# Performance work log

Hardware: AMD Instinct MI355X
Metric: run time of the kernel (lower is better)

## Reference

```python
import jax, jax.numpy as jnp
import numpy as np

N_MAP, N_ACT, B, E_PER, D = 131072, 1024, 16, 16384, 128
MAP_PER, ACT_PER = N_MAP // B, N_ACT // B
E = B * E_PER
EPS = 1e-5  # torch GroupNorm default eps


def _gn(x, g, b):
    # GroupNorm(1, C) on [N, C]: per-row normalization over channels
    m = jnp.mean(x, -1, keepdims=True)
    v = jnp.mean((x - m) ** 2, -1, keepdims=True)
    return (x - m) * jax.lax.rsqrt(v + EPS) * g + b


def _lin_gn(x, W, g, b, act=True):
    # LaneGCN Linear: nn.Linear(bias=False) -> GroupNorm(1, n_out) -> optional ReLU
    y = _gn(x @ W.T, g, b)
    return jax.nn.relu(y) if act else y


def setup_inputs() -> dict:
    key = jax.random.key(0)
    keys = iter(jax.random.split(key, 64))
    nrm = lambda shape, s=1.0: jax.random.normal(next(keys), shape, jnp.float32) * s
    uni = lambda shape, s=1.0: jax.random.uniform(next(keys), shape, jnp.float32) * s
    inp = {}
    inp['feat'] = nrm((N_MAP, D))
    inp['turn'] = nrm((N_MAP, 2))
    inp['control'] = uni((N_MAP,))
    inp['intersect'] = uni((N_MAP,))
    inp['map_ctrs'] = uni((N_MAP, 2), 100.0)
    inp['actors'] = nrm((N_ACT, D))
    inp['actor_ctrs'] = uni((N_ACT, 2), 100.0)
    # fixed within-scene edge list (stands in for the distance-threshold nonzero)
    rng = np.random.default_rng(0)
    hi = np.concatenate([rng.integers(b * MAP_PER, (b + 1) * MAP_PER, E_PER) for b in range(B)])
    wi = np.concatenate([rng.integers(b * ACT_PER, (b + 1) * ACT_PER, E_PER) for b in range(B)])
    inp['hi'] = jnp.asarray(hi, jnp.int32)
    inp['wi'] = jnp.asarray(wi, jnp.int32)
    # parameters
    W = lambda *s: nrm(s, 0.02)
    g_ = lambda *s: 1.0 + nrm(s, 0.05)
    b_ = lambda *s: nrm(s, 0.05)
    inp['meta_W'], inp['meta_g'], inp['meta_b'] = W(D, D + 4), g_(D), b_(D)
    inp['dW1'], inp['db1'] = W(2, D, 2), b_(2, D)
    inp['dW2'], inp['dg2'], inp['dbt2'] = W(2, D, D), g_(2, D), b_(2, D)
    inp['qW'], inp['qg'], inp['qb'] = W(2, D, D), g_(2, D), b_(2, D)
    inp['cW1'], inp['cg1'], inp['cb1'] = W(2, D, 3 * D), g_(2, D), b_(2, D)
    inp['cW2'] = W(2, D, D)
    inp['aW'] = W(2, D, D)
    inp['ng_g'], inp['ng_b'] = g_(2, D), b_(2, D)
    inp['lW'], inp['lg'], inp['lb'] = W(2, D, D), g_(2, D), b_(2, D)
    return inp


def reference(feat, turn, control, intersect, map_ctrs, actors, actor_ctrs, hi, wi,
              meta_W, meta_g, meta_b, dW1, db1, dW2, dg2, dbt2, qW, qg, qb,
              cW1, cg1, cb1, cW2, aW, ng_g, ng_b, lW, lg, lb):
    # meta fuse: concat(feat, turn, control, intersect) -> Linear+GN+ReLU
    meta = jnp.concatenate([feat, turn, control[:, None], intersect[:, None]], axis=1)
    feat = _lin_gn(meta, meta_W, meta_g, meta_b)
    for i in range(2):  # two Att blocks
        res = feat
        # dist branch: raw ctr offsets -> Linear(2,n_ctx)+ReLU -> Linear+GN+ReLU
        d = map_ctrs[hi] - actor_ctrs[wi]                       # [E, 2]
        d = jax.nn.relu(d @ dW1[i].T + db1[i])                  # [E, D]
        d = _lin_gn(d, dW2[i], dg2[i], dbt2[i])
        q = _lin_gn(feat[hi], qW[i], qg[i], qb[i])              # query on gathered agts
        c = jnp.concatenate([d, q, actors[wi]], axis=1)         # [E, 3D]
        c = _lin_gn(c, cW1[i], cg1[i], cb1[i])
        c = c @ cW2[i].T                                        # bias-free Linear
        a = feat @ aW[i].T                                      # self path, bias-free
        a = a.at[hi].add(c)                                     # scatter-add messages
        a = jax.nn.relu(_gn(a, ng_g[i], ng_b[i]))
        a = _lin_gn(a, lW[i], lg[i], lb[i], act=False)
        feat = jax.nn.relu(a + res)                             # use_relu=True
    return feat
```

## Files before the change

kernel.cpp:

```cpp
#include <hip/hip_runtime.h>
#include <stdint.h>

typedef unsigned short u16;
typedef __bf16 bf16x8 __attribute__((ext_vector_type(8)));
typedef float f32x4 __attribute__((ext_vector_type(4)));

#define MFMA(a, b, c) __builtin_amdgcn_mfma_f32_16x16x32_bf16(a, b, c, 0, 0, 0)

__device__ __forceinline__ u16 f2bf(float f) {
    union { float f; unsigned u; } v; v.f = f;
    unsigned r = v.u + 0x7fffu + ((v.u >> 16) & 1u);
    return (u16)(r >> 16);
}
__device__ __forceinline__ float bf2f(u16 h) {
    union { unsigned u; float f; } v; v.u = ((unsigned)h) << 16; return v.f;
}
__device__ __forceinline__ bf16x8 as_frag(uint4 u) {
    union { uint4 u; bf16x8 b; } v; v.u = u; return v.b;
}
__device__ __forceinline__ bf16x8 ldg_frag(const u16* p) {
    return as_frag(*reinterpret_cast<const uint4*>(p));
}
__device__ __forceinline__ int rowmap(int t, int i) {
    return 32 * (t >> 1) + 8 * (i >> 2) + 4 * (t & 1) + (i & 3);
}

template <int KT>
__device__ __forceinline__ void gemm_acc(const bf16x8* a, const u16* __restrict__ W, int ldw,
                                         f32x4* acc, int c16, int q4) {
#pragma unroll
    for (int n = 0; n < 8; n++) {
        const u16* wp = W + (size_t)(n * 16 + c16) * ldw + q4 * 8;
#pragma unroll
        for (int k = 0; k < KT; k++) {
            bf16x8 b = ldg_frag(wp + k * 32);
            acc[n] = MFMA(a[k], b, acc[n]);
        }
    }
}

__device__ __forceinline__ void gn_t(f32x4* acc, const float* __restrict__ gb, bool relu, int q4) {
    float s = 0.f, s2 = 0.f;
#pragma unroll
    for (int t = 0; t < 8; t++)
#pragma unroll
        for (int r = 0; r < 4; r++) { float x = acc[t][r]; s += x; s2 = fmaf(x, x, s2); }
    s += __shfl_xor(s, 16, 64); s += __shfl_xor(s, 32, 64);
    s2 += __shfl_xor(s2, 16, 64); s2 += __shfl_xor(s2, 32, 64);
    float mean = s * (1.f / 128.f);
    float var = fmaf(s2, 1.f / 128.f, -mean * mean);
    float rstd = rsqrtf(var + 1e-5f);
#pragma unroll
    for (int t = 0; t < 8; t++) {
        const float4* g4 = reinterpret_cast<const float4*>(gb + (t * 16 + q4 * 4) * 2);
        float4 p01 = g4[0], p23 = g4[1];
        float gv[4] = {p01.x, p01.z, p23.x, p23.z};
        float bv[4] = {p01.y, p01.w, p23.y, p23.w};
#pragma unroll
        for (int r = 0; r < 4; r++) {
            float y = fmaf((acc[t][r] - mean) * rstd, gv[r], bv[r]);
            acc[t][r] = relu ? fmaxf(y, 0.f) : y;
        }
    }
}

__device__ __forceinline__ bf16x8 pack_frag(f32x4 lo, f32x4 hi) {
    union { u16 s[8]; bf16x8 b; } t;
#pragma unroll
    for (int j = 0; j < 4; j++) { t.s[j] = f2bf(lo[j]); t.s[4 + j] = f2bf(hi[j]); }
    return t.b;
}

__device__ __forceinline__ void gn_c(f32x4* acc, const float* __restrict__ g,
                                     const float* __restrict__ b, bool relu, int c16) {
    float gs[8], bs[8];
#pragma unroll
    for (int n = 0; n < 8; n++) { gs[n] = g[n * 16 + c16]; bs[n] = b[n * 16 + c16]; }
#pragma unroll
    for (int r = 0; r < 4; r++) {
        float s = 0.f, s2 = 0.f;
#pragma unroll
        for (int n = 0; n < 8; n++) { float x = acc[n][r]; s += x; s2 = fmaf(x, x, s2); }
#pragma unroll
        for (int m = 1; m < 16; m <<= 1) { s += __shfl_xor(s, m, 64); s2 += __shfl_xor(s2, m, 64); }
        float mean = s * (1.f / 128.f);
        float var = fmaf(s2, 1.f / 128.f, -mean * mean);
        float rstd = rsqrtf(var + 1e-5f);
#pragma unroll
        for (int n = 0; n < 8; n++) {
            float y = fmaf((acc[n][r] - mean) * rstd, gs[n], bs[n]);
            acc[n][r] = relu ? fmaxf(y, 0.f) : y;
        }
    }
}

__global__ __launch_bounds__(256) void k_prep(
    const float* __restrict__ dW2s, const float* __restrict__ qWs, const float* __restrict__ cW1s,
    const float* __restrict__ cW2s, const float* __restrict__ aWs, const float* __restrict__ lWs,
    const float* __restrict__ actors, const float* __restrict__ metaW,
    const float* __restrict__ dW1s, const float* __restrict__ db1s,
    const float* __restrict__ dg2s, const float* __restrict__ dbt2s,
    const float* __restrict__ qgs, const float* __restrict__ qbs,
    const float* __restrict__ cg1s, const float* __restrict__ cb1s,
    u16* __restrict__ o_dW2p, u16* __restrict__ o_qW, u16* __restrict__ o_cW1p,
    u16* __restrict__ o_cW2, u16* __restrict__ o_aW, u16* __restrict__ o_lW,
    u16* __restrict__ o_actb, u16* __restrict__ o_mWf, float* __restrict__ o_mWe,
    float* __restrict__ o_dw1p, float* __restrict__ o_gb) {
    int idx = blockIdx.x * 256 + threadIdx.x;
    if (idx >= 412672) return;
    if (idx < 32768) {
        int i = idx >> 14, rem = idx & 16383, ro = rem >> 7, col = rem & 127;
        o_dW2p[idx] = f2bf(dW2s[i * 16384 + rowmap(ro >> 4, ro & 15) * 128 + col]);
    } else if (idx < 65536) {
        int j = idx - 32768; o_qW[j] = f2bf(qWs[j]);
    } else if (idx < 163840) {
        int j = idx - 65536, i = j / 49152, rem = j - i * 49152, ro = rem / 384, col = rem - ro * 384;
        o_cW1p[j] = f2bf(cW1s[i * 49152 + rowmap(ro >> 4, ro & 15) * 384 + col]);
    } else if (idx < 196608) { int j = idx - 163840; o_cW2[j] = f2bf(cW2s[j]); }
    else if (idx < 229376) { int j = idx - 196608; o_aW[j] = f2bf(aWs[j]); }
    else if (idx < 262144) { int j = idx - 229376; o_lW[j] = f2bf(lWs[j]); }
    else if (idx < 393216) { int j = idx - 262144; o_actb[j] = f2bf(actors[j]); }
    else if (idx < 409600) { int j = idx - 393216; o_mWf[j] = f2bf(metaW[(j >> 7) * 132 + (j & 127)]); }
    else if (idx < 410112) { int j = idx - 409600; o_mWe[j] = metaW[(j >> 2) * 132 + 128 + (j & 3)]; }
    else if (idx < 411136) {
        int j = idx - 410112, i = j >> 9, col = (j >> 2) & 127, t = j & 3;
        float v = (t == 0) ? dW1s[i * 256 + col * 2]
                : (t == 1) ? dW1s[i * 256 + col * 2 + 1]
                : (t == 2) ? db1s[i * 128 + col] : 0.f;
        o_dw1p[j] = v;
    } else {
        int j = idx - 411136;
        int tb = j >> 9, rem = j & 511, i = rem >> 8, q = rem & 255, o = q >> 1, f = q & 1;
        const float* gsrc = (tb == 0) ? dg2s : (tb == 1) ? qgs : cg1s;
        const float* bsrc = (tb == 0) ? dbt2s : (tb == 1) ? qbs : cb1s;
        int src = i * 128 + rowmap(o >> 4, o & 15);
        o_gb[j] = f ? bsrc[src] : gsrc[src];
    }
}

__global__ __launch_bounds__(256) void k_meta(
    const float* __restrict__ feat, const float* __restrict__ turn,
    const float* __restrict__ ctrl, const float* __restrict__ inter,
    const u16* __restrict__ mWf, const float* __restrict__ mWe,
    const float* __restrict__ g, const float* __restrict__ b, u16* __restrict__ out) {
    int lane = threadIdx.x & 63, wv = threadIdx.x >> 6;
    int c16 = lane & 15, q4 = lane >> 4;
    int m0 = (blockIdx.x * 4 + wv) * 16;
    bf16x8 a[4];
    const float* xr = feat + (size_t)(m0 + c16) * 128 + q4 * 8;
#pragma unroll
    for (int k = 0; k < 4; k++) {
        float4 u0 = *reinterpret_cast<const float4*>(xr + k * 32);
        float4 u1 = *reinterpret_cast<const float4*>(xr + k * 32 + 4);
        union { u16 s[8]; bf16x8 b; } t;
        t.s[0] = f2bf(u0.x); t.s[1] = f2bf(u0.y); t.s[2] = f2bf(u0.z); t.s[3] = f2bf(u0.w);
        t.s[4] = f2bf(u1.x); t.s[5] = f2bf(u1.y); t.s[6] = f2bf(u1.z); t.s[7] = f2bf(u1.w);
        a[k] = t.b;
    }
    f32x4 acc[8] = {};
    gemm_acc<4>(a, mWf, 128, acc, c16, q4);
#pragma unroll
    for (int r = 0; r < 4; r++) {
        int row = m0 + q4 * 4 + r;
        float t0 = turn[2 * row], t1 = turn[2 * row + 1];
        float cv = ctrl[row], iv = inter[row];
#pragma unroll
        for (int n = 0; n < 8; n++) {
            int col = n * 16 + c16;
            float4 we = reinterpret_cast<const float4*>(mWe)[col];
            acc[n][r] += t0 * we.x + t1 * we.y + cv * we.z + iv * we.w;
        }
    }
    gn_c(acc, g, b, true, c16);
#pragma unroll
    for (int r = 0; r < 4; r++) {
        size_t row = m0 + q4 * 4 + r;
#pragma unroll
        for (int n = 0; n < 8; n++) out[row * 128 + n * 16 + c16] = f2bf(acc[n][r]);
    }
}

__global__ __launch_bounds__(256) void k_nodeA(
    const u16* __restrict__ featb, const u16* __restrict__ qW, const u16* __restrict__ aW,
    const float* __restrict__ qg, const float* __restrict__ qb,
    u16* __restrict__ q_out, float* __restrict__ a_out) {
    int lane = threadIdx.x & 63, wv = threadIdx.x >> 6;
    int c16 = lane & 15, q4 = lane >> 4;
    int m0 = (blockIdx.x * 4 + wv) * 16;
    bf16x8 a[4];
    const u16* xr = featb + (size_t)(m0 + c16) * 128 + q4 * 8;
#pragma unroll
    for (int k = 0; k < 4; k++) a[k] = ldg_frag(xr + k * 32);
    f32x4 accq[8] = {}, acca[8] = {};
    gemm_acc<4>(a, qW, 128, accq, c16, q4);
    gemm_acc<4>(a, aW, 128, acca, c16, q4);
#pragma unroll
    for (int r = 0; r < 4; r++) {
        size_t row = m0 + q4 * 4 + r;
#pragma unroll
        for (int n = 0; n < 8; n++) a_out[row * 128 + n * 16 + c16] = acca[n][r];
    }
    gn_c(accq, qg, qb, true, c16);
#pragma unroll
    for (int r = 0; r < 4; r++) {
        size_t row = m0 + q4 * 4 + r;
#pragma unroll
        for (int n = 0; n < 8; n++) q_out[row * 128 + n * 16 + c16] = f2bf(accq[n][r]);
    }
}

__global__ __launch_bounds__(256) void k_edge(
    const int* __restrict__ hi, const int* __restrict__ wi,
    const float* __restrict__ mctr, const float* __restrict__ actr,
    const float* __restrict__ dw1p, const u16* __restrict__ dW2p,
    const float* __restrict__ gb_d2,
    const u16* __restrict__ q_node, const u16* __restrict__ actb,
    const u16* __restrict__ cW1p, const float* __restrict__ gb_c1,
    const u16* __restrict__ cW2, float* __restrict__ a_out) {
    int lane = threadIdx.x & 63, wv = threadIdx.x >> 6;
    int c16 = lane & 15, q4 = lane >> 4;
    int bid = (int)blockIdx.x;
    bid = (bid & 7) * 256 + (bid >> 3);
    int ebase = bid * 128 + wv * 32;
    int h0 = hi[ebase + c16], w0 = wi[ebase + c16];
    int h1 = hi[ebase + 16 + c16], w1 = wi[ebase + 16 + c16];
    float dx0 = mctr[2 * h0] - actr[2 * w0], dy0 = mctr[2 * h0 + 1] - actr[2 * w0 + 1];
    float dx1 = mctr[2 * h1] - actr[2 * w1], dy1 = mctr[2 * h1 + 1] - actr[2 * w1 + 1];
    bf16x8 bd0[4], bd1[4];
    const float4* w4p = reinterpret_cast<const float4*>(dw1p);
#pragma unroll
    for (int k = 0; k < 4; k++) {
        union { u16 s[8]; uint4 u; } t0, t1;
#pragma unroll
        for (int j = 0; j < 8; j++) {
            float4 w4 = w4p[k * 32 + q4 * 8 + j];
            t0.s[j] = f2bf(fmaxf(fmaf(dx0, w4.x, fmaf(dy0, w4.y, w4.z)), 0.f));
            t1.s[j] = f2bf(fmaxf(fmaf(dx1, w4.x, fmaf(dy1, w4.y, w4.z)), 0.f));
        }
        bd0[k] = as_frag(t0.u); bd1[k] = as_frag(t1.u);
    }
    f32x4 accA[8] = {}, accB[8] = {};
#pragma unroll
    for (int k = 0; k < 4; k++) {
#pragma unroll
        for (int t = 0; t < 8; t++) {
            bf16x8 a = ldg_frag(dW2p + (size_t)(t * 16 + c16) * 128 + k * 32 + q4 * 8);
            accA[t] = MFMA(a, bd0[k], accA[t]);
            accB[t] = MFMA(a, bd1[k], accB[t]);
        }
    }
    gn_t(accA, gb_d2, true, q4);
    gn_t(accB, gb_d2, true, q4);
    bf16x8 d2f0[4], d2f1[4];
#pragma unroll
    for (int k = 0; k < 4; k++) {
        d2f0[k] = pack_frag(accA[2 * k], accA[2 * k + 1]);
        d2f1[k] = pack_frag(accB[2 * k], accB[2 * k + 1]);
    }
    const u16* qr0 = q_node + (size_t)h0 * 128 + q4 * 8;
    const u16* qr1 = q_node + (size_t)h1 * 128 + q4 * 8;
    const u16* ar0 = actb + (size_t)w0 * 128 + q4 * 8;
    const u16* ar1 = actb + (size_t)w1 * 128 + q4 * 8;
    f32x4 cA[8] = {}, cB[8] = {};
#pragma unroll
    for (int k = 0; k < 12; k++) {
        bf16x8 b0 = (k < 4) ? d2f0[k] : (k < 8) ? ldg_frag(qr0 + (k - 4) * 32)
                                                : ldg_frag(ar0 + (k - 8) * 32);
        bf16x8 b1 = (k < 4) ? d2f1[k] : (k < 8) ? ldg_frag(qr1 + (k - 4) * 32)
                                                : ldg_frag(ar1 + (k - 8) * 32);
#pragma unroll
        for (int t = 0; t < 8; t++) {
            bf16x8 a = ldg_frag(cW1p + (size_t)(t * 16 + c16) * 384 + k * 32 + q4 * 8);
            cA[t] = MFMA(a, b0, cA[t]);
            cB[t] = MFMA(a, b1, cB[t]);
        }
    }
    gn_t(cA, gb_c1, true, q4);
    gn_t(cB, gb_c1, true, q4);
    bf16x8 ba0[4], ba1[4];
#pragma unroll
    for (int k = 0; k < 4; k++) {
        ba0[k] = pack_frag(cA[2 * k], cA[2 * k + 1]);
        ba1[k] = pack_frag(cB[2 * k], cB[2 * k + 1]);
    }
    f32x4 oA[8] = {}, oB[8] = {};
#pragma unroll
    for (int k = 0; k < 4; k++) {
#pragma unroll
        for (int n = 0; n < 8; n++) {
            bf16x8 b = ldg_frag(cW2 + (size_t)(n * 16 + c16) * 128 + k * 32 + q4 * 8);
            oA[n] = MFMA(ba0[k], b, oA[n]);
            oB[n] = MFMA(ba1[k], b, oB[n]);
        }
    }
#pragma unroll
    for (int r = 0; r < 4; r++) {
        int hr0 = hi[ebase + q4 * 4 + r];
        int hr1 = hi[ebase + 16 + q4 * 4 + r];
        float* dst0 = a_out + (size_t)hr0 * 128 + c16;
        float* dst1 = a_out + (size_t)hr1 * 128 + c16;
#pragma unroll
        for (int n = 0; n < 8; n++) {
            unsafeAtomicAdd(dst0 + n * 16, oA[n][r]);
            unsafeAtomicAdd(dst1 + n * 16, oB[n][r]);
        }
    }
}

__global__ __launch_bounds__(256) void k_nodeB(
    const float* __restrict__ a_in, const float* __restrict__ gg, const float* __restrict__ gb,
    const u16* __restrict__ lW, const float* __restrict__ lg, const float* __restrict__ lb,
    const u16* __restrict__ res, u16* __restrict__ out_bf, float* __restrict__ out_f32) {
    int lane = threadIdx.x & 63, wv = threadIdx.x >> 6;
    int c16 = lane & 15, q4 = lane >> 4;
    int m0 = (blockIdx.x * 4 + wv) * 16;
    const float* xr = a_in + (size_t)(m0 + c16) * 128 + q4 * 8;
    float x[32];
#pragma unroll
    for (int k = 0; k < 4; k++) {
        float4 u0 = *reinterpret_cast<const float4*>(xr + k * 32);
        float4 u1 = *reinterpret_cast<const float4*>(xr + k * 32 + 4);
        x[k * 8 + 0] = u0.x; x[k * 8 + 1] = u0.y; x[k * 8 + 2] = u0.z; x[k * 8 + 3] = u0.w;
        x[k * 8 + 4] = u1.x; x[k * 8 + 5] = u1.y; x[k * 8 + 6] = u1.z; x[k * 8 + 7] = u1.w;
    }
    float s = 0.f, s2 = 0.f;
#pragma unroll
    for (int t = 0; t < 32; t++) { s += x[t]; s2 = fmaf(x[t], x[t], s2); }
    s += __shfl_xor(s, 16, 64); s += __shfl_xor(s, 32, 64);
    s2 += __shfl_xor(s2, 16, 64); s2 += __shfl_xor(s2, 32, 64);
    float mean = s * (1.f / 128.f);
    float var = fmaf(s2, 1.f / 128.f, -mean * mean);
    float rstd = rsqrtf(var + 1e-5f);
    bf16x8 a[4];
#pragma unroll
    for (int k = 0; k < 4; k++) {
        float4 g0 = *reinterpret_cast<const float4*>(gg + k * 32 + q4 * 8);
        float4 g1 = *reinterpret_cast<const float4*>(gg + k * 32 + q4 * 8 + 4);
        float4 b0 = *reinterpret_cast<const float4*>(gb + k * 32 + q4 * 8);
        float4 b1 = *reinterpret_cast<const float4*>(gb + k * 32 + q4 * 8 + 4);
        float gv[8] = {g0.x, g0.y, g0.z, g0.w, g1.x, g1.y, g1.z, g1.w};
        float bv[8] = {b0.x, b0.y, b0.z, b0.w, b1.x, b1.y, b1.z, b1.w};
        union { u16 s[8]; bf16x8 b; } t;
#pragma unroll
        for (int j = 0; j < 8; j++) {
            float y = fmaf((x[k * 8 + j] - mean) * rstd, gv[j], bv[j]);
            t.s[j] = f2bf(fmaxf(y, 0.f));
        }
        a[k] = t.b;
    }
    f32x4 acc[8] = {};
    gemm_acc<4>(a, lW, 128, acc, c16, q4);
    gn_c(acc, lg, lb, false, c16);
#pragma unroll
    for (int r = 0; r < 4; r++) {
        size_t row = m0 + q4 * 4 + r;
#pragma unroll
        for (int n = 0; n < 8; n++) {
            int col = n * 16 + c16;
            float y = acc[n][r] + bf2f(res[row * 128 + col]);
            y = fmaxf(y, 0.f);
            if (out_bf) out_bf[row * 128 + col] = f2bf(y);
            else out_f32[row * 128 + col] = y;
        }
    }
}

extern "C" void kernel_launch(void* const* d_in, const int* in_sizes, int n_in,
                              void* d_out, int out_size, void* d_ws, size_t ws_size,
                              hipStream_t stream) {
    const float* feat = (const float*)d_in[0];
    const float* turn = (const float*)d_in[1];
    const float* ctrl = (const float*)d_in[2];
    const float* inter = (const float*)d_in[3];
    const float* mctr = (const float*)d_in[4];
    const float* actors = (const float*)d_in[5];
    const float* actr = (const float*)d_in[6];
    const int* hi = (const int*)d_in[7];
    const int* wi = (const int*)d_in[8];
    const float* metaW = (const float*)d_in[9];
    const float* metag = (const float*)d_in[10];
    const float* metab = (const float*)d_in[11];
    const float* dW1 = (const float*)d_in[12];
    const float* db1 = (const float*)d_in[13];
    const float* dW2 = (const float*)d_in[14];
    const float* dg2 = (const float*)d_in[15];
    const float* dbt2 = (const float*)d_in[16];
    const float* qW = (const float*)d_in[17];
    const float* qg = (const float*)d_in[18];
    const float* qb = (const float*)d_in[19];
    const float* cW1 = (const float*)d_in[20];
    const float* cg1 = (const float*)d_in[21];
    const float* cb1 = (const float*)d_in[22];
    const float* cW2 = (const float*)d_in[23];
    const float* aW = (const float*)d_in[24];
    const float* ngg = (const float*)d_in[25];
    const float* ngb = (const float*)d_in[26];
    const float* lW = (const float*)d_in[27];
    const float* lg = (const float*)d_in[28];
    const float* lb = (const float*)d_in[29];

    char* ws = (char*)d_ws;
    u16* feat0 = (u16*)(ws);
    u16* feat1 = (u16*)(ws + 33554432);
    u16* qbuf = (u16*)(ws + 67108864);
    u16* actb = (u16*)(ws + 100663296);
    u16* wmWf = (u16*)(ws + 100925440);
    u16* wdW2p = (u16*)(ws + 100958208);
    u16* wqW = (u16*)(ws + 101023744);
    u16* wcW1p = (u16*)(ws + 101089280);
    u16* wcW2 = (u16*)(ws + 101285888);
    u16* waW = (u16*)(ws + 101351424);
    u16* wlW = (u16*)(ws + 101416960);
    float* wmWe = (float*)(ws + 101482496);
    float* wdw1p = (float*)(ws + 101484544);
    float* gball = (float*)(ws + 101488640);
    float* abuf = (float*)d_out;

    k_prep<<<1613, 256, 0, stream>>>(dW2, qW, cW1, cW2, aW, lW, actors, metaW, dW1, db1,
                                     dg2, dbt2, qg, qb, cg1, cb1,
                                     wdW2p, wqW, wcW1p, wcW2, waW, wlW, actb, wmWf, wmWe,
                                     wdw1p, gball);
    k_meta<<<2048, 256, 0, stream>>>(feat, turn, ctrl, inter, wmWf, wmWe, metag, metab, feat0);
    for (int i = 0; i < 2; i++) {
        const u16* fcur = i ? feat1 : feat0;
        k_nodeA<<<2048, 256, 0, stream>>>(fcur, wqW + i * 16384, waW + i * 16384,
                                          qg + i * 128, qb + i * 128, qbuf, abuf);
        k_edge<<<2048, 256, 0, stream>>>(hi, wi, mctr, actr, wdw1p + i * 512, wdW2p + i * 16384,
                                         gball + i * 256, qbuf, actb,
                                         wcW1p + i * 49152, gball + 1024 + i * 256,
                                         wcW2 + i * 16384, abuf);
        k_nodeB<<<2048, 256, 0, stream>>>(abuf, ngg + i * 128, ngb + i * 128, wlW + i * 16384,
                                          lg + i * 128, lb + i * 128, fcur,
                                          i ? nullptr : feat1, i ? (float*)d_out : nullptr);
    }
}
```

Baseline: 798.7 us.

## Stage edge-kernel weight matrices in swizzled LDS instead of global loads

The edge kernel now copies the dW2, cW1 (in three 128-column slices) and cW2 weight tiles into two 32 KB shared-memory buffers with an XOR swizzle, and reads MFMA operands from LDS instead of issuing per-wave global loads. The gathered q and actor rows are prefetched into registers at kernel start so their latency overlaps the weight staging and the dist MLP. This cuts repeated L2/global traffic for weights shared by all four waves. The cost is 64 KB of LDS per block, which lowers occupancy, plus several block-wide barriers.

```diff
diff --git a/kernel.cpp b/kernel.cpp
--- a/kernel.cpp
+++ b/kernel.cpp
@@ -23,6 +23,20 @@
 }
 __device__ __forceinline__ int rowmap(int t, int i) {
     return 32 * (t >> 1) + 8 * (i >> 2) + 4 * (t & 1) + (i & 3);
+}
+
+template <int SRC_LDU>
+__device__ __forceinline__ void stage128(const u16* __restrict__ src, u16* dst, int tid, int nt) {
+    for (int c = tid; c < 2048; c += nt) {
+        int row = c >> 4, j = c & 15;
+        int js = (j & 8) | ((j ^ row) & 7);
+        *reinterpret_cast<uint4*>(dst + row * 128 + js * 8) =
+            *reinterpret_cast<const uint4*>(src + row * SRC_LDU + j * 8);
+    }
+}
+__device__ __forceinline__ bf16x8 lds_w(const u16* base, int row, int byteoff) {
+    int off = row * 256 + (byteoff ^ ((row & 7) << 4));
+    return as_frag(*reinterpret_cast<const uint4*>(reinterpret_cast<const char*>(base) + off));
 }
 
 template <int KT>
@@ -217,13 +231,30 @@
     const u16* __restrict__ q_node, const u16* __restrict__ actb,
     const u16* __restrict__ cW1p, const float* __restrict__ gb_c1,
     const u16* __restrict__ cW2, float* __restrict__ a_out) {
-    int lane = threadIdx.x & 63, wv = threadIdx.x >> 6;
+    __shared__ u16 s0[16384];
+    __shared__ u16 s1[16384];
+    int tid = threadIdx.x;
+    int lane = tid & 63, wv = tid >> 6;
     int c16 = lane & 15, q4 = lane >> 4;
     int bid = (int)blockIdx.x;
     bid = (bid & 7) * 256 + (bid >> 3);
     int ebase = bid * 128 + wv * 32;
     int h0 = hi[ebase + c16], w0 = wi[ebase + c16];
     int h1 = hi[ebase + 16 + c16], w1 = wi[ebase + 16 + c16];
+    stage128<128>(dW2p, s0, tid, 256);
+    stage128<384>(cW1p, s1, tid, 256);
+    bf16x8 qf0[4], qf1[4], af0[4], af1[4];
+    {
+        const u16* qr0 = q_node + (size_t)h0 * 128 + q4 * 8;
+        const u16* qr1 = q_node + (size_t)h1 * 128 + q4 * 8;
+        const u16* ar0 = actb + (size_t)w0 * 128 + q4 * 8;
+        const u16* ar1 = actb + (size_t)w1 * 128 + q4 * 8;
+#pragma unroll
+        for (int k = 0; k < 4; k++) {
+            qf0[k] = ldg_frag(qr0 + k * 32); qf1[k] = ldg_frag(qr1 + k * 32);
+            af0[k] = ldg_frag(ar0 + k * 32); af1[k] = ldg_frag(ar1 + k * 32);
+        }
+    }
     float dx0 = mctr[2 * h0] - actr[2 * w0], dy0 = mctr[2 * h0 + 1] - actr[2 * w0 + 1];
     float dx1 = mctr[2 * h1] - actr[2 * w1], dy1 = mctr[2 * h1 + 1] - actr[2 * w1 + 1];
     bf16x8 bd0[4], bd1[4];
@@ -239,16 +270,16 @@
         }
         bd0[k] = as_frag(t0.u); bd1[k] = as_frag(t1.u);
     }
+    __syncthreads();
     f32x4 accA[8] = {}, accB[8] = {};
 #pragma unroll
-    for (int k = 0; k < 4; k++) {
+    for (int k = 0; k < 4; k++)
 #pragma unroll
         for (int t = 0; t < 8; t++) {
-            bf16x8 a = ldg_frag(dW2p + (size_t)(t * 16 + c16) * 128 + k * 32 + q4 * 8);
+            bf16x8 a = lds_w(s0, t * 16 + c16, k * 64 + q4 * 16);
             accA[t] = MFMA(a, bd0[k], accA[t]);
             accB[t] = MFMA(a, bd1[k], accB[t]);
         }
-    }
     gn_t(accA, gb_d2, true, q4);
     gn_t(accB, gb_d2, true, q4);
     bf16x8 d2f0[4], d2f1[4];
@@ -257,24 +288,37 @@
         d2f0[k] = pack_frag(accA[2 * k], accA[2 * k + 1]);
         d2f1[k] = pack_frag(accB[2 * k], accB[2 * k + 1]);
     }
-    const u16* qr0 = q_node + (size_t)h0 * 128 + q4 * 8;
-    const u16* qr1 = q_node + (size_t)h1 * 128 + q4 * 8;
-    const u16* ar0 = actb + (size_t)w0 * 128 + q4 * 8;
-    const u16* ar1 = actb + (size_t)w1 * 128 + q4 * 8;
     f32x4 cA[8] = {}, cB[8] = {};
 #pragma unroll
-    for (int k = 0; k < 12; k++) {
-        bf16x8 b0 = (k < 4) ? d2f0[k] : (k < 8) ? ldg_frag(qr0 + (k - 4) * 32)
-                                                : ldg_frag(ar0 + (k - 8) * 32);
-        bf16x8 b1 = (k < 4) ? d2f1[k] : (k < 8) ? ldg_frag(qr1 + (k - 4) * 32)
-                                                : ldg_frag(ar1 + (k - 8) * 32);
+    for (int k = 0; k < 4; k++)
 #pragma unroll
         for (int t = 0; t < 8; t++) {
-            bf16x8 a = ldg_frag(cW1p + (size_t)(t * 16 + c16) * 384 + k * 32 + q4 * 8);
-            cA[t] = MFMA(a, b0, cA[t]);
-            cB[t] = MFMA(a, b1, cB[t]);
-        }
-    }
+            bf16x8 a = lds_w(s1, t * 16 + c16, k * 64 + q4 * 16);
+            cA[t] = MFMA(a, d2f0[k], cA[t]);
+            cB[t] = MFMA(a, d2f1[k], cB[t]);
+        }
+    __syncthreads();
+    stage128<384>(cW1p + 128, s0, tid, 256);
+    stage128<384>(cW1p + 256, s1, tid, 256);
+    __syncthreads();
+#pragma unroll
+    for (int k = 0; k < 4; k++)
+#pragma unroll
+        for (int t = 0; t < 8; t++) {
+            bf16x8 a = lds_w(s0, t * 16 + c16, k * 64 + q4 * 16);
+            cA[t] = MFMA(a, qf0[k], cA[t]);
+            cB[t] = MFMA(a, qf1[k], cB[t]);
+        }
+#pragma unroll
+    for (int k = 0; k < 4; k++)
+#pragma unroll
+        for (int t = 0; t < 8; t++) {
+            bf16x8 a = lds_w(s1, t * 16 + c16, k * 64 + q4 * 16);
+            cA[t] = MFMA(a, af0[k], cA[t]);
+            cB[t] = MFMA(a, af1[k], cB[t]);
+        }
+    __syncthreads();
+    stage128<128>(cW2, s0, tid, 256);
     gn_t(cA, gb_c1, true, q4);
     gn_t(cB, gb_c1, true, q4);
     bf16x8 ba0[4], ba1[4];
@@ -283,16 +327,16 @@
         ba0[k] = pack_frag(cA[2 * k], cA[2 * k + 1]);
         ba1[k] = pack_frag(cB[2 * k], cB[2 * k + 1]);
     }
+    __syncthreads();
     f32x4 oA[8] = {}, oB[8] = {};
 #pragma unroll
-    for (int k = 0; k < 4; k++) {
+    for (int k = 0; k < 4; k++)
 #pragma unroll
         for (int n = 0; n < 8; n++) {
-            bf16x8 b = ldg_frag(cW2 + (size_t)(n * 16 + c16) * 128 + k * 32 + q4 * 8);
+            bf16x8 b = lds_w(s0, n * 16 + c16, k * 64 + q4 * 16);
             oA[n] = MFMA(ba0[k], b, oA[n]);
             oB[n] = MFMA(ba1[k], b, oB[n]);
         }
-    }
 #pragma unroll
     for (int r = 0; r < 4; r++) {
         int hr0 = hi[ebase + q4 * 4 + r];
```

Result: faster. 672.1 us (-15.9%).
